# Performance work log

Hardware: AMD Instinct MI355X
Metric: run time of the kernel (lower is better)

Reference implementation:

```python
import jax, jax.numpy as jnp
import numpy as np

L, B, S, H, NH, F = 4, 2, 1024, 1024, 16, 4096
DH = H // NH

def setup_inputs() -> dict:
    key = jax.random.key(0)
    ks = jax.random.split(key, 16)
    std = 0.02
    return {
        'x': jax.random.normal(ks[0], (B, S, H), jnp.float32),
        'attention_mask': jnp.ones((B, S, S), jnp.float32),
        'wq': jax.random.normal(ks[1], (L, H, H), jnp.float32) * std,
        'bq': jnp.zeros((L, H), jnp.float32),
        'wk': jax.random.normal(ks[2], (L, H, H), jnp.float32) * std,
        'bk': jnp.zeros((L, H), jnp.float32),
        'wv': jax.random.normal(ks[3], (L, H, H), jnp.float32) * std,
        'bv': jnp.zeros((L, H), jnp.float32),
        'wo_attn': jax.random.normal(ks[4], (L, H, H), jnp.float32) * std,
        'bo_attn': jnp.zeros((L, H), jnp.float32),
        'alpha_attn': jax.random.uniform(ks[5], (L,), jnp.float32) * 0.1,
        'wi': jax.random.normal(ks[6], (L, H, F), jnp.float32) * std,
        'bi': jnp.zeros((L, F), jnp.float32),
        'wo_ffn': jax.random.normal(ks[7], (L, F, H), jnp.float32) * std,
        'bo_ffn': jnp.zeros((L, H), jnp.float32),
        'alpha_ffn': jax.random.uniform(ks[8], (L,), jnp.float32) * 0.1,
    }

def _heads(t):
    # [B,S,H] -> [B,NH,S,DH]
    return t.reshape(B, S, NH, DH).transpose(0, 2, 1, 3)

def reference(x, attention_mask, wq, bq, wk, bk, wv, bv, wo_attn, bo_attn,
              alpha_attn, wi, bi, wo_ffn, bo_ffn, alpha_ffn):
    # additive mask: (1 - mask) * -10000, broadcast over heads
    adder = (1.0 - attention_mask)[:, None, :, :] * -10000.0  # [B,1,S,S]
    scale = 1.0 / jnp.sqrt(jnp.asarray(DH, x.dtype))
    for l in range(L):
        q = _heads(x @ wq[l] + bq[l])
        k = _heads(x @ wk[l] + bk[l])
        v = _heads(x @ wv[l] + bv[l])
        scores = jnp.einsum('bhqd,bhkd->bhqk', q, k) * scale + adder
        probs = jax.nn.softmax(scores, axis=-1)
        ctx = jnp.einsum('bhqk,bhkd->bhqd', probs, v)
        ctx = ctx.transpose(0, 2, 1, 3).reshape(B, S, H)
        attn_out = ctx @ wo_attn[l] + bo_attn[l]
        x = x + alpha_attn[l] * attn_out  # rezero residual
        inter = jax.nn.gelu(x @ wi[l] + bi[l], approximate=True)
        ffn_out = inter @ wo_ffn[l] + bo_ffn[l]
        x = x + alpha_ffn[l] * ffn_out  # rezero residual
    return x
```

## Files before the change

### kernel.cpp

```cpp
#include <hip/hip_runtime.h>
#include <cstdint>

#define B_  2
#define S_  1024
#define H_  1024
#define NH_ 16
#define DH_ 64
#define F_  4096
#define L_  4
#define M_  (B_*S_)
#define BHS_ (B_*NH_*S_)

typedef __bf16 bf16;
typedef __bf16 bf16x8 __attribute__((ext_vector_type(8)));
typedef __bf16 bf16x4 __attribute__((ext_vector_type(4)));
typedef __bf16 bf16x2 __attribute__((ext_vector_type(2)));
typedef float  f32x4  __attribute__((ext_vector_type(4)));

__device__ __forceinline__ void async_ld16(void* lds, const void* g) {
  auto* lp = reinterpret_cast<__attribute__((address_space(3))) unsigned int*>(
      reinterpret_cast<uintptr_t>(lds));
  const auto* gp = reinterpret_cast<const __attribute__((address_space(1))) unsigned int*>(
      reinterpret_cast<uintptr_t>(g));
  __builtin_amdgcn_global_load_lds(gp, lp, 16, 0, 0);
}

__device__ __forceinline__ float gelu_tanh(float x) {
  float u = 0.7978845608028654f * (x + 0.044715f * x * x * x);
  u = fminf(fmaxf(u, -15.f), 15.f);
  float e = __builtin_amdgcn_exp2f(u * 2.8853900817779268f);
  return 0.5f * x * (1.f + (e - 1.f) / (e + 1.f));
}

__global__ __launch_bounds__(256) void transpose_cvt(
    const float* __restrict__ src, bf16* __restrict__ dst, int K, int N,
    size_t src_z, size_t dst_z) {
  __shared__ float t[32][33];
  const int n0 = blockIdx.x * 32, k0 = blockIdx.y * 32;
  const size_t so = (size_t)blockIdx.z * src_z;
  const size_t dz = (size_t)blockIdx.z * dst_z;
  const int x = threadIdx.x, y = threadIdx.y;
  #pragma unroll
  for (int i = 0; i < 32; i += 8)
    t[y + i][x] = src[so + (size_t)(k0 + y + i) * N + n0 + x];
  __syncthreads();
  #pragma unroll
  for (int i = 0; i < 32; i += 8)
    dst[dz + (size_t)(n0 + y + i) * K + k0 + x] = (bf16)t[x][y + i];
}

__global__ __launch_bounds__(256) void mask_cvt(
    const float4* __restrict__ m, bf16x4* __restrict__ out) {
  const int i = blockIdx.x * 256 + (int)threadIdx.x;
  const float c2 = -10000.f * 1.44269504088896f;
  float4 v = m[i];
  bf16x4 o;
  o[0] = (bf16)((1.f - v.x) * c2);
  o[1] = (bf16)((1.f - v.y) * c2);
  o[2] = (bf16)((1.f - v.z) * c2);
  o[3] = (bf16)((1.f - v.w) * c2);
  out[i] = o;
}

__global__ __launch_bounds__(256) void init_x_kernel(
    const float4* __restrict__ x, float4* __restrict__ xf, bf16x4* __restrict__ xb) {
  int i = blockIdx.x * 256 + threadIdx.x;
  float4 v = x[i];
  xf[i] = v;
  bf16x4 b;
  b[0] = (bf16)v.x; b[1] = (bf16)v.y; b[2] = (bf16)v.z; b[3] = (bf16)v.w;
  xb[i] = b;
}

__device__ __forceinline__ void gemm_core(
    const bf16* __restrict__ A, const bf16* __restrict__ Bt, int ld, int kLen,
    int m0, int n0, bf16* As, bf16* Bs, f32x4 (&acc)[4][4]) {
  const int tid = (int)threadIdx.x;
  const int w = tid >> 6, l = tid & 63;
  const int lr = l & 15, lg = l >> 4;
  const int wm = w >> 1, wn = w & 1;
  const int srow = l >> 2;
  const int scol = (l & 3) * 8;

  const bf16* ag = A  + (size_t)(m0 + w * 32 + srow) * ld + scol;
  const bf16* bg = Bt + (size_t)(n0 + w * 32 + srow) * ld + scol;
  const int soff = (w * 32) * 32;

  auto stage = [&](int buf, int kk) {
    bf16* ad = As + buf * 4096 + soff;
    bf16* bd = Bs + buf * 4096 + soff;
    async_ld16(ad,           ag + kk);
    async_ld16(ad + 16 * 32, ag + kk + (size_t)16 * ld);
    async_ld16(bd,           bg + kk);
    async_ld16(bd + 16 * 32, bg + kk + (size_t)16 * ld);
  };

  stage(0, 0);
  __syncthreads();
  int cur = 0;
  for (int k0 = 0; k0 < kLen; k0 += 32) {
    if (k0 + 32 < kLen) stage(cur ^ 1, k0 + 32);
    const bf16* Ab = As + cur * 4096;
    const bf16* Bb = Bs + cur * 4096;
    bf16x8 af[4], bv[4];
    #pragma unroll
    for (int i = 0; i < 4; ++i)
      af[i] = *(const bf16x8*)(Ab + (wm * 64 + i * 16 + lr) * 32 + lg * 8);
    #pragma unroll
    for (int i = 0; i < 4; ++i)
      bv[i] = *(const bf16x8*)(Bb + (wn * 64 + i * 16 + lr) * 32 + lg * 8);
    #pragma unroll
    for (int i = 0; i < 4; ++i)
      #pragma unroll
      for (int j = 0; j < 4; ++j)
        acc[i][j] = __builtin_amdgcn_mfma_f32_16x16x32_bf16(af[i], bv[j], acc[i][j], 0, 0, 0);
    __syncthreads();
    cur ^= 1;
  }
}

template <int MODE>
__global__ __launch_bounds__(256) void gemm128_kernel(
    const bf16* __restrict__ A, const bf16* __restrict__ Bt,
    const float* __restrict__ bias, bf16* __restrict__ outb,
    float* __restrict__ outf, const float* __restrict__ alphap,
    float* __restrict__ part, int N, int K, int kSlice) {
  __shared__ __align__(16) bf16 As[2 * 128 * 32];
  __shared__ __align__(16) bf16 Bs[2 * 128 * 32];
  const int m0 = blockIdx.y * 128, n0 = blockIdx.x * 128;
  const int z = blockIdx.z;
  const f32x4 z4 = {0.f, 0.f, 0.f, 0.f};
  f32x4 acc[4][4];
  #pragma unroll
  for (int i = 0; i < 4; ++i)
    #pragma unroll
    for (int j = 0; j < 4; ++j) acc[i][j] = z4;

  gemm_core(A + (size_t)z * kSlice, Bt + (size_t)z * kSlice, K, kSlice,
            m0, n0, As, Bs, acc);

  const int tid = (int)threadIdx.x;
  const int w = tid >> 6, l = tid & 63;
  const int lr = l & 15, lg = l >> 4;
  const int wm = w >> 1, wn = w & 1;
  float alpha = 0.f;
  if (MODE == 2) alpha = *alphap;
  const size_t pbase = (MODE == 3) ? (size_t)z * M_ * (size_t)N : 0;
  #pragma unroll
  for (int i = 0; i < 4; ++i) {
    const int row0 = m0 + wm * 64 + i * 16 + lg * 4;
    #pragma unroll
    for (int j = 0; j < 4; ++j) {
      const int col = n0 + wn * 64 + j * 16 + lr;
      const float bvx = (MODE == 3) ? 0.f : bias[col];
      #pragma unroll
      for (int r = 0; r < 4; ++r) {
        const size_t idx = (size_t)(row0 + r) * N + col;
        float v = acc[i][j][r] + bvx;
        if (MODE == 3) {
          part[pbase + idx] = v;
        } else if (MODE == 1) {
          outb[idx] = (bf16)gelu_tanh(v);
        } else if (MODE == 2) {
          float xn = outf[idx] + alpha * v;
          outf[idx] = xn;
          outb[idx] = (bf16)xn;
        } else {
          outb[idx] = (bf16)v;
        }
      }
    }
  }
}

__global__ __launch_bounds__(256) void reduce_residual(
    const float4* __restrict__ part, const float* __restrict__ bias,
    const float* __restrict__ alphap, float4* __restrict__ xf,
    bf16x4* __restrict__ xb) {
  const int i = blockIdx.x * 256 + (int)threadIdx.x;
  const int nper = M_ * H_ / 4;
  float4 s = part[i];
  #pragma unroll
  for (int zz = 1; zz < 4; ++zz) {
    float4 p = part[i + (size_t)zz * nper];
    s.x += p.x; s.y += p.y; s.z += p.z; s.w += p.w;
  }
  const int col = (i * 4) & (H_ - 1);
  const float4 b4 = *(const float4*)(bias + col);
  const float a = *alphap;
  float4 xv = xf[i];
  xv.x += a * (s.x + b4.x);
  xv.y += a * (s.y + b4.y);
  xv.z += a * (s.z + b4.z);
  xv.w += a * (s.w + b4.w);
  xf[i] = xv;
  bf16x4 bb;
  bb[0] = (bf16)xv.x; bb[1] = (bf16)xv.y; bb[2] = (bf16)xv.z; bb[3] = (bf16)xv.w;
  xb[i] = bb;
}

__global__ __launch_bounds__(256) void gemm_qkv_kernel(
    const bf16* __restrict__ A,
    const bf16* __restrict__ WtQ, const bf16* __restrict__ WtK, const bf16* __restrict__ WtV,
    const float* __restrict__ bq, const float* __restrict__ bk, const float* __restrict__ bvv,
    bf16* __restrict__ qo, bf16* __restrict__ ko, bf16* __restrict__ vt) {
  __shared__ __align__(16) bf16 As[2 * 128 * 32];
  __shared__ __align__(16) bf16 Bs[2 * 128 * 32];
  const int z = blockIdx.z;
  const bf16* Bt = (z == 0) ? WtQ : (z == 1) ? WtK : WtV;
  const float* bias = (z == 0) ? bq : (z == 1) ? bk : bvv;
  const int m0 = blockIdx.y * 128, n0 = blockIdx.x * 128;
  const f32x4 z4 = {0.f, 0.f, 0.f, 0.f};
  f32x4 acc[4][4];
  #pragma unroll
  for (int i = 0; i < 4; ++i)
    #pragma unroll
    for (int j = 0; j < 4; ++j) acc[i][j] = z4;

  gemm_core(A, Bt, H_, H_, m0, n0, As, Bs, acc);

  const int tid = (int)threadIdx.x;
  const int w = tid >> 6, l = tid & 63;
  const int lr = l & 15, lg = l >> 4;
  const int wm = w >> 1, wn = w & 1;
  if (z < 2) {
    bf16* out = z ? ko : qo;
    #pragma unroll
    for (int i = 0; i < 4; ++i) {
      const int row0 = m0 + wm * 64 + i * 16 + lg * 4;
      #pragma unroll
      for (int j = 0; j < 4; ++j) {
        const int col = n0 + wn * 64 + j * 16 + lr;
        const float bvx = bias[col];
        #pragma unroll
        for (int r = 0; r < 4; ++r)
          out[(size_t)(row0 + r) * H_ + col] = (bf16)(acc[i][j][r] + bvx);
      }
    }
  } else {
    #pragma unroll
    for (int i = 0; i < 4; ++i) {
      const int row0 = m0 + wm * 64 + i * 16 + lg * 4;
      const int bb = row0 >> 10, ss = row0 & (S_ - 1);
      #pragma unroll
      for (int j = 0; j < 4; ++j) {
        const int col = n0 + wn * 64 + j * 16 + lr;
        const float bvx = bias[col];
        const int hh = col >> 6, dd = col & 63;
        bf16x4 pk;
        #pragma unroll
        for (int r = 0; r < 4; ++r) pk[r] = (bf16)(acc[i][j][r] + bvx);
        *(bf16x4*)(vt + (((size_t)(bb * NH_ + hh) * DH_ + dd) << 10) + ss) = pk;
      }
    }
  }
}

__global__ __launch_bounds__(256) void attn_kernel5(
    const bf16* __restrict__ Q, const bf16* __restrict__ Kb,
    const bf16* __restrict__ Vt, const bf16* __restrict__ madd,
    float* __restrict__ pctx, float* __restrict__ pm, float* __restrict__ pl) {
  const int tid = (int)threadIdx.x;
  const int w = tid >> 6, l = tid & 63;
  const int lr = l & 15, lg = l >> 4;
  const int r7 = lr & 7;
  const int h = blockIdx.y;
  const int b = blockIdx.z >> 1, half = blockIdx.z & 1;
  const int q0 = blockIdx.x * 64 + w * 16;
  const int kvbase = half * (S_ / 2);

  __shared__ __align__(16) bf16 Kt[2][64 * 64];
  __shared__ __align__(16) bf16 Vs[2][64 * 64];
  __shared__ unsigned int Pu[4][16][36];

  const bf16* qp = Q + ((size_t)(b * S_ + q0 + lr)) * H_ + h * DH_;
  const bf16x8 qa0 = *(const bf16x8*)(qp + lg * 8);
  const bf16x8 qa1 = *(const bf16x8*)(qp + 32 + lg * 8);

  const f32x4 z4 = {0.f, 0.f, 0.f, 0.f};
  f32x4 acc[4];
  #pragma unroll
  for (int dt = 0; dt < 4; ++dt) acc[dt] = z4;
  float mrow = -1e30f, ssum = 0.f;

  const bf16* Kbase = Kb + ((size_t)b * S_) * H_ + h * DH_;
  const bf16* Vbase = Vt + ((size_t)(b * NH_ + h)) * DH_ * S_;
  const bf16* Mb = madd + ((size_t)(b * S_ + q0 + lr)) * S_;

  const float c1 = 0.125f * 1.44269504088896f;
  const float THR = 10.f;

  const int sub = l >> 3;
  const int cs  = ((l & 7) ^ sub) * 8;
  auto stage = [&](int buf, int kv) {
    #pragma unroll
    for (int j = 0; j < 2; ++j) {
      const int rbase = w * 16 + j * 8;
      async_ld16(&Kt[buf][rbase * 64],
                 Kbase + (size_t)(kv + rbase + sub) * H_ + cs);
      async_ld16(&Vs[buf][rbase * 64],
                 Vbase + (size_t)(rbase + sub) * S_ + kv + cs);
    }
  };

  stage(0, kvbase);
  __syncthreads();
  int cur = 0;
  #pragma unroll 1
  for (int it = 0; it < 8; ++it) {
    const int kv0 = kvbase + it * 64;
    if (it < 7) stage(cur ^ 1, kv0 + 64);
    const bf16* Kc = &Kt[cur][0];
    const bf16* Vc = &Vs[cur][0];
    bf16x8 kf0[4], kf1[4];
    bf16x4 mk[4];
    #pragma unroll
    for (int t = 0; t < 4; ++t) {
      kf0[t] = *(const bf16x8*)(Kc + (t * 16 + lr) * 64 + ((lg ^ r7) * 8));
      kf1[t] = *(const bf16x8*)(Kc + (t * 16 + lr) * 64 + (((4 + lg) ^ r7) * 8));
      mk[t] = *(const bf16x4*)(Mb + kv0 + t * 16 + lg * 4);
    }
    f32x4 st[4];
    __builtin_amdgcn_s_setprio(1);
    #pragma unroll
    for (int t = 0; t < 4; ++t) {
      f32x4 s = __builtin_amdgcn_mfma_f32_16x16x32_bf16(kf0[t], qa0, z4, 0, 0, 0);
      st[t] = __builtin_amdgcn_mfma_f32_16x16x32_bf16(kf1[t], qa1, s, 0, 0, 0);
    }
    __builtin_amdgcn_s_setprio(0);
    float sv[4][4];
    #pragma unroll
    for (int t = 0; t < 4; ++t)
      #pragma unroll
      for (int r = 0; r < 4; ++r)
        sv[t][r] = st[t][r] * c1 + (float)mk[t][r];
    float nm = sv[0][0];
    #pragma unroll
    for (int t = 0; t < 4; ++t)
      #pragma unroll
      for (int r = 0; r < 4; ++r) nm = fmaxf(nm, sv[t][r]);
    nm = fmaxf(nm, __shfl_xor(nm, 16));
    nm = fmaxf(nm, __shfl_xor(nm, 32));
    if (__any(nm > mrow + THR)) {
      float newm = fmaxf(mrow, nm);
      float f = __builtin_amdgcn_exp2f(mrow - newm);
      mrow = newm;
      ssum *= f;
      #pragma unroll
      for (int dt = 0; dt < 4; ++dt)
        #pragma unroll
        for (int r = 0; r < 4; ++r) acc[dt][r] *= f;
    }
    float p[4][4];
    float ps = 0.f;
    #pragma unroll
    for (int t = 0; t < 4; ++t)
      #pragma unroll
      for (int r = 0; r < 4; ++r) {
        p[t][r] = __builtin_amdgcn_exp2f(sv[t][r] - mrow);
        ps += p[t][r];
      }
    ps += __shfl_xor(ps, 16);
    ps += __shfl_xor(ps, 32);
    ssum += ps;
    #pragma unroll
    for (int t = 0; t < 4; ++t)
      #pragma unroll
      for (int hh = 0; hh < 2; ++hh) {
        union { bf16x2 v; unsigned int u; } pk;
        pk.v[0] = (bf16)p[t][2 * hh];
        pk.v[1] = (bf16)p[t][2 * hh + 1];
        Pu[w][lr][8 * t + 2 * lg + hh] = pk.u;
      }
    const bf16x8 pf0 = *(const bf16x8*)&Pu[w][lr][4 * lg];
    const bf16x8 pf1 = *(const bf16x8*)&Pu[w][lr][16 + 4 * lg];
    __builtin_amdgcn_s_setprio(1);
    #pragma unroll
    for (int dt = 0; dt < 4; ++dt) {
      bf16x8 vb0 = *(const bf16x8*)(Vc + (dt * 16 + lr) * 64 + ((lg ^ r7) * 8));
      acc[dt] = __builtin_amdgcn_mfma_f32_16x16x32_bf16(vb0, pf0, acc[dt], 0, 0, 0);
    }
    #pragma unroll
    for (int dt = 0; dt < 4; ++dt) {
      bf16x8 vb1 = *(const bf16x8*)(Vc + (dt * 16 + lr) * 64 + (((4 + lg) ^ r7) * 8));
      acc[dt] = __builtin_amdgcn_mfma_f32_16x16x32_bf16(vb1, pf1, acc[dt], 0, 0, 0);
    }
    __builtin_amdgcn_s_setprio(0);
    __syncthreads();
    cur ^= 1;
  }
  const int gq = (b * NH_ + h) * S_ + q0 + lr;
  const size_t rowi = (size_t)half * BHS_ + gq;
  #pragma unroll
  for (int dt = 0; dt < 4; ++dt)
    *(f32x4*)(pctx + rowi * 64 + dt * 16 + lg * 4) = acc[dt];
  if (lg == 0) { pm[rowi] = mrow; pl[rowi] = ssum; }
}

__global__ __launch_bounds__(256) void attn_combine(
    const float4* __restrict__ pctx, const float* __restrict__ pm,
    const float* __restrict__ pl, bf16* __restrict__ Ctx) {
  const int i = blockIdx.x * 256 + (int)threadIdx.x;
  const int q = i >> 4, d4 = (i & 15) * 4;
  const float m0 = pm[q], m1 = pm[BHS_ + q];
  const float l0 = pl[q], l1 = pl[BHS_ + q];
  const float M = fmaxf(m0, m1);
  const float a0 = __builtin_amdgcn_exp2f(m0 - M);
  const float a1 = __builtin_amdgcn_exp2f(m1 - M);
  const float inv = 1.f / (l0 * a0 + l1 * a1);
  const float w0 = a0 * inv, w1 = a1 * inv;
  const float4 c0 = pctx[i];
  const float4 c1 = pctx[(size_t)BHS_ * 16 + i];
  bf16x4 o;
  o[0] = (bf16)(c0.x * w0 + c1.x * w1);
  o[1] = (bf16)(c0.y * w0 + c1.y * w1);
  o[2] = (bf16)(c0.z * w0 + c1.z * w1);
  o[3] = (bf16)(c0.w * w0 + c1.w * w1);
  const int bb = q >> 14, hh = (q >> 10) & (NH_ - 1), s = q & (S_ - 1);
  *(bf16x4*)(Ctx + ((size_t)(bb * S_ + s)) * H_ + hh * DH_ + d4) = o;
}

extern "C" void kernel_launch(void* const* d_in, const int* in_sizes, int n_in,
                              void* d_out, int out_size, void* d_ws, size_t ws_size,
                              hipStream_t stream) {
  (void)in_sizes; (void)n_in; (void)out_size; (void)ws_size;
  const float* x    = (const float*)d_in[0];
  const float* mask = (const float*)d_in[1];
  const float* wq   = (const float*)d_in[2];
  const float* bq   = (const float*)d_in[3];
  const float* wk   = (const float*)d_in[4];
  const float* bk   = (const float*)d_in[5];
  const float* wv   = (const float*)d_in[6];
  const float* bv   = (const float*)d_in[7];
  const float* wo   = (const float*)d_in[8];
  const float* bo   = (const float*)d_in[9];
  const float* aat  = (const float*)d_in[10];
  const float* wi   = (const float*)d_in[11];
  const float* bi   = (const float*)d_in[12];
  const float* wf   = (const float*)d_in[13];
  const float* bf_  = (const float*)d_in[14];
  const float* afn  = (const float*)d_in[15];

  char* ws = (char*)d_ws;
  size_t o = 0;
  bf16* WtQKV = (bf16*)(ws + o); o += (size_t)L_ * 3 * H_ * H_ * 2;
  bf16* WtO = (bf16*)(ws + o); o += (size_t)L_ * H_ * H_ * 2;
  bf16* WtI = (bf16*)(ws + o); o += (size_t)L_ * H_ * F_ * 2;
  bf16* WtF = (bf16*)(ws + o); o += (size_t)L_ * F_ * H_ * 2;
  bf16* madd = (bf16*)(ws + o); o += (size_t)B_ * S_ * S_ * 2;
  bf16* xb  = (bf16*)(ws + o); o += (size_t)M_ * H_ * 2;
  bf16* qb  = (bf16*)(ws + o); o += (size_t)M_ * H_ * 2;
  bf16* kbf = (bf16*)(ws + o); o += (size_t)M_ * H_ * 2;
  bf16* vt  = (bf16*)(ws + o); o += (size_t)M_ * H_ * 2;
  bf16* ctx = (bf16*)(ws + o); o += (size_t)M_ * H_ * 2;
  bf16* itm = (bf16*)(ws + o); o += (size_t)M_ * F_ * 2;
  float* part = (float*)(ws + o); o += (size_t)4 * M_ * H_ * 4;
  float* pctx = part;
  float* pm   = part + (size_t)2 * BHS_ * 64;
  float* pl   = pm + (size_t)2 * BHS_;

  float* xf = (float*)d_out;

  const dim3 tb(32, 8);
  const size_t HH = (size_t)H_ * H_;
  transpose_cvt<<<dim3(H_/32, H_/32, L_), tb, 0, stream>>>(wq, WtQKV,        H_, H_, HH, 3*HH);
  transpose_cvt<<<dim3(H_/32, H_/32, L_), tb, 0, stream>>>(wk, WtQKV + HH,   H_, H_, HH, 3*HH);
  transpose_cvt<<<dim3(H_/32, H_/32, L_), tb, 0, stream>>>(wv, WtQKV + 2*HH, H_, H_, HH, 3*HH);
  transpose_cvt<<<dim3(H_/32, H_/32, L_), tb, 0, stream>>>(wo, WtO, H_, H_, HH, HH);
  transpose_cvt<<<dim3(F_/32, H_/32, L_), tb, 0, stream>>>(wi, WtI, H_, F_, (size_t)H_*F_, (size_t)H_*F_);
  transpose_cvt<<<dim3(H_/32, F_/32, L_), tb, 0, stream>>>(wf, WtF, F_, H_, (size_t)F_*H_, (size_t)F_*H_);
  mask_cvt<<<dim3((B_*S_*S_/4)/256), 256, 0, stream>>>((const float4*)mask, (bf16x4*)madd);
  init_x_kernel<<<dim3((M_ * H_ / 4) / 256), 256, 0, stream>>>(
      (const float4*)x, (float4*)xf, (bf16x4*)xb);

  for (int l = 0; l < L_; ++l) {
    gemm_qkv_kernel<<<dim3(H_/128, M_/128, 3), 256, 0, stream>>>(
        xb, WtQKV + (size_t)l * 3 * HH, WtQKV + (size_t)l * 3 * HH + HH,
        WtQKV + (size_t)l * 3 * HH + 2 * HH,
        bq + l * H_, bk + l * H_, bv + l * H_, qb, kbf, vt);
    attn_kernel5<<<dim3(S_/64, NH_, B_*2), 256, 0, stream>>>(
        qb, kbf, vt, madd, pctx, pm, pl);
    attn_combine<<<dim3((BHS_ * 16) / 256), 256, 0, stream>>>(
        (const float4*)pctx, pm, pl, ctx);
    gemm128_kernel<3><<<dim3(H_/128, M_/128, 4), 256, 0, stream>>>(
        ctx, WtO + (size_t)l * HH, nullptr, nullptr, nullptr, nullptr,
        part, H_, H_, H_ / 4);
    reduce_residual<<<dim3((M_ * H_ / 4) / 256), 256, 0, stream>>>(
        (const float4*)part, bo + l * H_, aat + l, (float4*)xf, (bf16x4*)xb);
    gemm128_kernel<1><<<dim3(F_/128, M_/128), 256, 0, stream>>>(
        xb, WtI + (size_t)l * H_ * F_, bi + l * F_, itm, nullptr, nullptr,
        nullptr, F_, H_, H_);
    gemm128_kernel<3><<<dim3(H_/128, M_/128, 4), 256, 0, stream>>>(
        itm, WtF + (size_t)l * F_ * H_, nullptr, nullptr, nullptr, nullptr,
        part, H_, F_, F_ / 4);
    reduce_residual<<<dim3((M_ * H_ / 4) / 256), 256, 0, stream>>>(
        (const float4*)part, bf_ + l * H_, afn + l, (float4*)xf, (bf16x4*)xb);
  }
}
```

Measured before the change: 679.1 us.

## Drop split-KV attention and combine kernel; retile QKV GEMM to 128x64

Attention now handles the full KV range in one block per query tile and normalizes the output directly to bf16 context. This removes the split-KV partial buffers and the separate combine kernel. The QKV projection now uses a fused 128x64-tile kernel over the concatenated weight matrix (48 column tiles), which raises the block count. The trade-off is that attention runs with half as many blocks (512), each doing twice the serial KV iterations. Unused MODE 2 and MODE 0 epilogue paths are also removed from the generic GEMM.

```diff
diff --git a/kernel.cpp b/kernel.cpp
--- a/kernel.cpp
+++ b/kernel.cpp
@@ -9,7 +9,6 @@
 #define F_  4096
 #define L_  4
 #define M_  (B_*S_)
-#define BHS_ (B_*NH_*S_)
 
 typedef __bf16 bf16;
 typedef __bf16 bf16x8 __attribute__((ext_vector_type(8)));
@@ -123,7 +122,6 @@
 __global__ __launch_bounds__(256) void gemm128_kernel(
     const bf16* __restrict__ A, const bf16* __restrict__ Bt,
     const float* __restrict__ bias, bf16* __restrict__ outb,
-    float* __restrict__ outf, const float* __restrict__ alphap,
     float* __restrict__ part, int N, int K, int kSlice) {
   __shared__ __align__(16) bf16 As[2 * 128 * 32];
   __shared__ __align__(16) bf16 Bs[2 * 128 * 32];
@@ -143,8 +141,6 @@
   const int w = tid >> 6, l = tid & 63;
   const int lr = l & 15, lg = l >> 4;
   const int wm = w >> 1, wn = w & 1;
-  float alpha = 0.f;
-  if (MODE == 2) alpha = *alphap;
   const size_t pbase = (MODE == 3) ? (size_t)z * M_ * (size_t)N : 0;
   #pragma unroll
   for (int i = 0; i < 4; ++i) {
@@ -159,14 +155,8 @@
         float v = acc[i][j][r] + bvx;
         if (MODE == 3) {
           part[pbase + idx] = v;
-        } else if (MODE == 1) {
+        } else {
           outb[idx] = (bf16)gelu_tanh(v);
-        } else if (MODE == 2) {
-          float xn = outf[idx] + alpha * v;
-          outf[idx] = xn;
-          outb[idx] = (bf16)xn;
-        } else {
-          outb[idx] = (bf16)v;
         }
       }
     }
@@ -199,38 +189,73 @@
   xb[i] = bb;
 }
 
-__global__ __launch_bounds__(256) void gemm_qkv_kernel(
-    const bf16* __restrict__ A,
-    const bf16* __restrict__ WtQ, const bf16* __restrict__ WtK, const bf16* __restrict__ WtV,
-    const float* __restrict__ bq, const float* __restrict__ bk, const float* __restrict__ bvv,
+__global__ __launch_bounds__(256) void gemm_qkv64(
+    const bf16* __restrict__ A, const bf16* __restrict__ Wt,
+    const float* __restrict__ bq, const float* __restrict__ bk,
+    const float* __restrict__ bvv,
     bf16* __restrict__ qo, bf16* __restrict__ ko, bf16* __restrict__ vt) {
   __shared__ __align__(16) bf16 As[2 * 128 * 32];
-  __shared__ __align__(16) bf16 Bs[2 * 128 * 32];
-  const int z = blockIdx.z;
-  const bf16* Bt = (z == 0) ? WtQ : (z == 1) ? WtK : WtV;
-  const float* bias = (z == 0) ? bq : (z == 1) ? bk : bvv;
-  const int m0 = blockIdx.y * 128, n0 = blockIdx.x * 128;
-  const f32x4 z4 = {0.f, 0.f, 0.f, 0.f};
-  f32x4 acc[4][4];
-  #pragma unroll
-  for (int i = 0; i < 4; ++i)
-    #pragma unroll
-    for (int j = 0; j < 4; ++j) acc[i][j] = z4;
-
-  gemm_core(A, Bt, H_, H_, m0, n0, As, Bs, acc);
-
+  __shared__ __align__(16) bf16 Bs[2 * 64 * 32];
   const int tid = (int)threadIdx.x;
   const int w = tid >> 6, l = tid & 63;
   const int lr = l & 15, lg = l >> 4;
   const int wm = w >> 1, wn = w & 1;
-  if (z < 2) {
-    bf16* out = z ? ko : qo;
+  const int srow = l >> 2, scol = (l & 3) * 8;
+  const int m0 = blockIdx.y * 128, n0 = blockIdx.x * 64;
+
+  const bf16* ag = A  + (size_t)(m0 + w * 32 + srow) * H_ + scol;
+  const bf16* bg = Wt + (size_t)(n0 + w * 16 + srow) * H_ + scol;
+  const int aoff = (w * 32) * 32;
+  const int boff = (w * 16) * 32;
+
+  auto stage = [&](int buf, int kk) {
+    bf16* ad = As + buf * 4096 + aoff;
+    bf16* bd = Bs + buf * 2048 + boff;
+    async_ld16(ad,           ag + kk);
+    async_ld16(ad + 16 * 32, ag + kk + (size_t)16 * H_);
+    async_ld16(bd,           bg + kk);
+  };
+
+  const f32x4 z4 = {0.f, 0.f, 0.f, 0.f};
+  f32x4 acc[4][2];
+  #pragma unroll
+  for (int i = 0; i < 4; ++i)
+    #pragma unroll
+    for (int j = 0; j < 2; ++j) acc[i][j] = z4;
+
+  stage(0, 0);
+  __syncthreads();
+  int cur = 0;
+  for (int k0 = 0; k0 < H_; k0 += 32) {
+    if (k0 + 32 < H_) stage(cur ^ 1, k0 + 32);
+    const bf16* Ab = As + cur * 4096;
+    const bf16* Bb = Bs + cur * 2048;
+    bf16x8 af[4], bv[2];
+    #pragma unroll
+    for (int i = 0; i < 4; ++i)
+      af[i] = *(const bf16x8*)(Ab + (wm * 64 + i * 16 + lr) * 32 + lg * 8);
+    #pragma unroll
+    for (int j = 0; j < 2; ++j)
+      bv[j] = *(const bf16x8*)(Bb + (wn * 32 + j * 16 + lr) * 32 + lg * 8);
+    #pragma unroll
+    for (int i = 0; i < 4; ++i)
+      #pragma unroll
+      for (int j = 0; j < 2; ++j)
+        acc[i][j] = __builtin_amdgcn_mfma_f32_16x16x32_bf16(af[i], bv[j], acc[i][j], 0, 0, 0);
+    __syncthreads();
+    cur ^= 1;
+  }
+
+  if (n0 < 2048) {
+    bf16* out = (n0 < 1024) ? qo : ko;
+    const float* bias = (n0 < 1024) ? bq : bk;
+    const int nl = n0 & 1023;
     #pragma unroll
     for (int i = 0; i < 4; ++i) {
       const int row0 = m0 + wm * 64 + i * 16 + lg * 4;
       #pragma unroll
-      for (int j = 0; j < 4; ++j) {
-        const int col = n0 + wn * 64 + j * 16 + lr;
+      for (int j = 0; j < 2; ++j) {
+        const int col = nl + wn * 32 + j * 16 + lr;
         const float bvx = bias[col];
         #pragma unroll
         for (int r = 0; r < 4; ++r)
@@ -238,15 +263,15 @@
       }
     }
   } else {
+    const int hh = (n0 >> 6) - 32;
     #pragma unroll
     for (int i = 0; i < 4; ++i) {
       const int row0 = m0 + wm * 64 + i * 16 + lg * 4;
       const int bb = row0 >> 10, ss = row0 & (S_ - 1);
       #pragma unroll
-      for (int j = 0; j < 4; ++j) {
-        const int col = n0 + wn * 64 + j * 16 + lr;
-        const float bvx = bias[col];
-        const int hh = col >> 6, dd = col & 63;
+      for (int j = 0; j < 2; ++j) {
+        const int dd = wn * 32 + j * 16 + lr;
+        const float bvx = bvv[hh * 64 + dd];
         bf16x4 pk;
         #pragma unroll
         for (int r = 0; r < 4; ++r) pk[r] = (bf16)(acc[i][j][r] + bvx);
@@ -256,18 +281,16 @@
   }
 }
 
-__global__ __launch_bounds__(256) void attn_kernel5(
+__global__ __launch_bounds__(256) void attn_kernel6(
     const bf16* __restrict__ Q, const bf16* __restrict__ Kb,
     const bf16* __restrict__ Vt, const bf16* __restrict__ madd,
-    float* __restrict__ pctx, float* __restrict__ pm, float* __restrict__ pl) {
+    bf16* __restrict__ Ctx) {
   const int tid = (int)threadIdx.x;
   const int w = tid >> 6, l = tid & 63;
   const int lr = l & 15, lg = l >> 4;
   const int r7 = lr & 7;
-  const int h = blockIdx.y;
-  const int b = blockIdx.z >> 1, half = blockIdx.z & 1;
+  const int h = blockIdx.y, b = blockIdx.z;
   const int q0 = blockIdx.x * 64 + w * 16;
-  const int kvbase = half * (S_ / 2);
 
   __shared__ __align__(16) bf16 Kt[2][64 * 64];
   __shared__ __align__(16) bf16 Vs[2][64 * 64];
@@ -303,13 +326,13 @@
     }
   };
 
-  stage(0, kvbase);
+  stage(0, 0);
   __syncthreads();
   int cur = 0;
   #pragma unroll 1
-  for (int it = 0; it < 8; ++it) {
-    const int kv0 = kvbase + it * 64;
-    if (it < 7) stage(cur ^ 1, kv0 + 64);
+  for (int it = 0; it < 16; ++it) {
+    const int kv0 = it * 64;
+    if (it < 15) stage(cur ^ 1, kv0 + 64);
     const bf16* Kc = &Kt[cur][0];
     const bf16* Vc = &Vs[cur][0];
     bf16x8 kf0[4], kf1[4];
@@ -389,35 +412,15 @@
     __syncthreads();
     cur ^= 1;
   }
-  const int gq = (b * NH_ + h) * S_ + q0 + lr;
-  const size_t rowi = (size_t)half * BHS_ + gq;
-  #pragma unroll
-  for (int dt = 0; dt < 4; ++dt)
-    *(f32x4*)(pctx + rowi * 64 + dt * 16 + lg * 4) = acc[dt];
-  if (lg == 0) { pm[rowi] = mrow; pl[rowi] = ssum; }
-}
-
-__global__ __launch_bounds__(256) void attn_combine(
-    const float4* __restrict__ pctx, const float* __restrict__ pm,
-    const float* __restrict__ pl, bf16* __restrict__ Ctx) {
-  const int i = blockIdx.x * 256 + (int)threadIdx.x;
-  const int q = i >> 4, d4 = (i & 15) * 4;
-  const float m0 = pm[q], m1 = pm[BHS_ + q];
-  const float l0 = pl[q], l1 = pl[BHS_ + q];
-  const float M = fmaxf(m0, m1);
-  const float a0 = __builtin_amdgcn_exp2f(m0 - M);
-  const float a1 = __builtin_amdgcn_exp2f(m1 - M);
-  const float inv = 1.f / (l0 * a0 + l1 * a1);
-  const float w0 = a0 * inv, w1 = a1 * inv;
-  const float4 c0 = pctx[i];
-  const float4 c1 = pctx[(size_t)BHS_ * 16 + i];
-  bf16x4 o;
-  o[0] = (bf16)(c0.x * w0 + c1.x * w1);
-  o[1] = (bf16)(c0.y * w0 + c1.y * w1);
-  o[2] = (bf16)(c0.z * w0 + c1.z * w1);
-  o[3] = (bf16)(c0.w * w0 + c1.w * w1);
-  const int bb = q >> 14, hh = (q >> 10) & (NH_ - 1), s = q & (S_ - 1);
-  *(bf16x4*)(Ctx + ((size_t)(bb * S_ + s)) * H_ + hh * DH_ + d4) = o;
+  const float inv = 1.f / ssum;
+  bf16* cp = Ctx + ((size_t)(b * S_ + q0 + lr)) * H_ + h * DH_;
+  #pragma unroll
+  for (int dt = 0; dt < 4; ++dt) {
+    bf16x4 o;
+    #pragma unroll
+    for (int r = 0; r < 4; ++r) o[r] = (bf16)(acc[dt][r] * inv);
+    *(bf16x4*)(cp + dt * 16 + lg * 4) = o;
+  }
 }
 
 extern "C" void kernel_launch(void* const* d_in, const int* in_sizes, int n_in,
@@ -455,9 +458,6 @@
   bf16* ctx = (bf16*)(ws + o); o += (size_t)M_ * H_ * 2;
   bf16* itm = (bf16*)(ws + o); o += (size_t)M_ * F_ * 2;
   float* part = (float*)(ws + o); o += (size_t)4 * M_ * H_ * 4;
-  float* pctx = part;
-  float* pm   = part + (size_t)2 * BHS_ * 64;
-  float* pl   = pm + (size_t)2 * BHS_;
 
   float* xf = (float*)d_out;
 
@@ -474,25 +474,19 @@
       (const float4*)x, (float4*)xf, (bf16x4*)xb);
 
   for (int l = 0; l < L_; ++l) {
-    gemm_qkv_kernel<<<dim3(H_/128, M_/128, 3), 256, 0, stream>>>(
-        xb, WtQKV + (size_t)l * 3 * HH, WtQKV + (size_t)l * 3 * HH + HH,
-        WtQKV + (size_t)l * 3 * HH + 2 * HH,
+    gemm_qkv64<<<dim3(48, M_/128), 256, 0, stream>>>(
+        xb, WtQKV + (size_t)l * 3 * HH,
         bq + l * H_, bk + l * H_, bv + l * H_, qb, kbf, vt);
-    attn_kernel5<<<dim3(S_/64, NH_, B_*2), 256, 0, stream>>>(
-        qb, kbf, vt, madd, pctx, pm, pl);
-    attn_combine<<<dim3((BHS_ * 16) / 256), 256, 0, stream>>>(
-        (const float4*)pctx, pm, pl, ctx);
+    attn_kernel6<<<dim3(S_/64, NH_, B_), 256, 0, stream>>>(
+        qb, kbf, vt, madd, ctx);
     gemm128_kernel<3><<<dim3(H_/128, M_/128, 4), 256, 0, stream>>>(
-        ctx, WtO + (size_t)l * HH, nullptr, nullptr, nullptr, nullptr,
-        part, H_, H_, H_ / 4);
+        ctx, WtO + (size_t)l * HH, nullptr, nullptr, part, H_, H_, H_ / 4);
     reduce_residual<<<dim3((M_ * H_ / 4) / 256), 256, 0, stream>>>(
         (const float4*)part, bo + l * H_, aat + l, (float4*)xf, (bf16x4*)xb);
     gemm128_kernel<1><<<dim3(F_/128, M_/128), 256, 0, stream>>>(
-        xb, WtI + (size_t)l * H_ * F_, bi + l * F_, itm, nullptr, nullptr,
-        nullptr, F_, H_, H_);
+        xb, WtI + (size_t)l * H_ * F_, bi + l * F_, itm, nullptr, F_, H_, H_);
     gemm128_kernel<3><<<dim3(H_/128, M_/128, 4), 256, 0, stream>>>(
-        itm, WtF + (size_t)l * F_ * H_, nullptr, nullptr, nullptr, nullptr,
-        part, H_, F_, F_ / 4);
+        itm, WtF + (size_t)l * F_ * H_, nullptr, nullptr, part, H_, F_, F_ / 4);
     reduce_residual<<<dim3((M_ * H_ / 4) / 256), 256, 0, stream>>>(
         (const float4*)part, bf_ + l * H_, afn + l, (float4*)xf, (bf16x4*)xb);
   }
```

Result: faster. 656.8 us (-3.3%).
